# Kernel optimization log

Hardware: AMD Instinct MI355X
Metric: run time of the kernel (lower is better)

## Reference

```python
import jax, jax.numpy as jnp
import numpy as np

HIDDEN = 1024
HEADS = 16
HEAD_DIM = HIDDEN // HEADS
GAMMA = 0.5
B, S = 2, 2048


def setup_inputs() -> dict:
    key = jax.random.key(0)
    ks = jax.random.split(key, 9)
    sc = 1.0 / np.sqrt(HIDDEN)
    x = jax.random.normal(ks[0], (B, S, HIDDEN), dtype=jnp.float32)
    attn_mask = jnp.zeros((S, S), dtype=bool)  # True = masked; all-False here
    Wq = jax.random.normal(ks[1], (HIDDEN, HIDDEN), dtype=jnp.float32) * sc
    bq = jnp.zeros((HIDDEN,), dtype=jnp.float32)
    Wk = jax.random.normal(ks[2], (HIDDEN, HIDDEN), dtype=jnp.float32) * sc
    bk = jnp.zeros((HIDDEN,), dtype=jnp.float32)
    Wv = jax.random.normal(ks[3], (HIDDEN, HIDDEN), dtype=jnp.float32) * sc
    bv = jnp.zeros((HIDDEN,), dtype=jnp.float32)
    Wo = jax.random.normal(ks[4], (HIDDEN, HIDDEN), dtype=jnp.float32) * sc
    bo = jnp.zeros((HIDDEN,), dtype=jnp.float32)
    return {"x": x, "attn_mask": attn_mask, "Wq": Wq, "bq": bq,
            "Wk": Wk, "bk": bk, "Wv": Wv, "bv": bv, "Wo": Wo, "bo": bo}


def reference(x, attn_mask, Wq, bq, Wk, bk, Wv, bv, Wo, bo):
    Bn, Sn, _ = x.shape
    # projections (torch Linear: x @ W.T + b), reshape to [B, H, S, Dh]
    def proj(W, b):
        y = x @ W.T + b
        return y.reshape(Bn, Sn, HEADS, HEAD_DIM).transpose(0, 2, 1, 3)
    q, k, v = proj(Wq, bq), proj(Wk, bk), proj(Wv, bv)
    scores = jnp.einsum('bhqd,bhkd->bhqk', q, k) / np.sqrt(HEAD_DIM)
    # diversity bias: cosine similarity of raw x (F.normalize eps=1e-12)
    normed = x / jnp.maximum(jnp.linalg.norm(x, axis=-1, keepdims=True), 1e-12)
    sim = jnp.einsum('bqd,bkd->bqk', normed, normed)
    scores = scores - GAMMA * sim[:, None, :, :]
    scores = jnp.where(attn_mask[None, None, :, :], -jnp.inf, scores)
    probs = jax.nn.softmax(scores, axis=-1)
    ctx = jnp.einsum('bhqk,bhkd->bhqd', probs, v)
    ctx = ctx.transpose(0, 2, 1, 3).reshape(Bn, Sn, HIDDEN)
    return ctx @ Wo.T + bo
```

## Files before the change

kernel.cpp:

```cpp
#include <hip/hip_runtime.h>

#define HID 1024
#define SEQ 2048
#define NB 2
#define NH 16
#define HD 64

#define C1 0.1803368801111204f
#define C2 0.7213475204444817f

typedef __attribute__((ext_vector_type(8))) short bf16x8;
typedef __attribute__((ext_vector_type(8))) unsigned short u16x8;
typedef __attribute__((ext_vector_type(4))) float f32x4;

__device__ __forceinline__ unsigned short f2bf(float f) {
  unsigned u = __builtin_bit_cast(unsigned, f);
  u += 0x7fffu + ((u >> 16) & 1u);
  return (unsigned short)(u >> 16);
}
__device__ __forceinline__ float bf2f(unsigned short u) {
  return __builtin_bit_cast(float, ((unsigned)u) << 16);
}

#define GLOAD16(gsrc, ldst)                                                     \
  __builtin_amdgcn_global_load_lds(                                             \
      (const __attribute__((address_space(1))) void*)(gsrc),                    \
      (__attribute__((address_space(3))) void*)(ldst), 16, 0, 0)

__global__ __launch_bounds__(256) void convert_w_kernel(
    const float* __restrict__ Wq, const float* __restrict__ Wk,
    const float* __restrict__ Wv, const float* __restrict__ Wo,
    unsigned short* __restrict__ Wb) {
  int i = blockIdx.x * 256 + threadIdx.x;
  const int per = (HID * HID) / 8;
  int m = i / per;
  const float* sp = (m == 0) ? Wq : (m == 1) ? Wk : (m == 2) ? Wv : Wo;
  int j = (i - m * per) * 8;
  const float4* p = reinterpret_cast<const float4*>(sp + j);
  float4 a = p[0], b = p[1];
  u16x8 o;
  o[0] = f2bf(a.x); o[1] = f2bf(a.y); o[2] = f2bf(a.z); o[3] = f2bf(a.w);
  o[4] = f2bf(b.x); o[5] = f2bf(b.y); o[6] = f2bf(b.z); o[7] = f2bf(b.w);
  *reinterpret_cast<u16x8*>(Wb + (size_t)i * 8) = o;
}

__global__ __launch_bounds__(256) void rownorm_kernel(
    const float* __restrict__ x, unsigned short* __restrict__ xb,
    unsigned short* __restrict__ nxb) {
  int row = blockIdx.x, tid = threadIdx.x;
  const float4 v = reinterpret_cast<const float4*>(x + (size_t)row * HID)[tid];
  float ss = v.x * v.x + v.y * v.y + v.z * v.z + v.w * v.w;
#pragma unroll
  for (int off = 32; off; off >>= 1) ss += __shfl_xor(ss, off, 64);
  __shared__ float wsum[4];
  if ((tid & 63) == 0) wsum[tid >> 6] = ss;
  __syncthreads();
  float tot = wsum[0] + wsum[1] + wsum[2] + wsum[3];
  float inv = 1.0f / fmaxf(sqrtf(tot), 1e-12f);
  ushort4 a, b;
  a.x = f2bf(v.x); a.y = f2bf(v.y); a.z = f2bf(v.z); a.w = f2bf(v.w);
  b.x = f2bf(v.x * inv); b.y = f2bf(v.y * inv);
  b.z = f2bf(v.z * inv); b.w = f2bf(v.w * inv);
  reinterpret_cast<ushort4*>(xb  + (size_t)row * HID)[tid] = a;
  reinterpret_cast<ushort4*>(nxb + (size_t)row * HID)[tid] = b;
}

template <int MODE>
__global__ __launch_bounds__(256) void gemm_nt(
    const unsigned short* __restrict__ A, long strideA,
    const unsigned short* __restrict__ B, long strideB,
    void* __restrict__ Cv, long strideC, int ldc,
    int M, int N, int K,
    const float* __restrict__ b0, const float* __restrict__ b1,
    const float* __restrict__ b2, const unsigned char* __restrict__ mask) {
  __shared__ __align__(16) unsigned short As[128 * 32];
  __shared__ __align__(16) unsigned short Bs[128 * 32];
  int tid = threadIdx.x, lane = tid & 63, wid = tid >> 6;
  int g = lane >> 4, lr = lane & 15;
  int wr = wid >> 1, wc = wid & 1;
  int m0 = blockIdx.y * 128, n0 = blockIdx.x * 128;
  const unsigned short* Ab = A + (size_t)blockIdx.z * strideA
      + (size_t)(m0 + wid * 32 + (lane >> 2)) * K + (lane & 3) * 8;
  const unsigned short* Bb = B + (size_t)blockIdx.z * strideB
      + (size_t)(n0 + wid * 32 + (lane >> 2)) * K + (lane & 3) * 8;
  unsigned short* la = As + wid * 1024;
  unsigned short* lb = Bs + wid * 1024;
  f32x4 acc[4][4] = {};
  for (int k0 = 0; k0 < K; k0 += 32) {
    GLOAD16(Ab + k0, la);
    GLOAD16(Ab + 16 * K + k0, la + 512);
    GLOAD16(Bb + k0, lb);
    GLOAD16(Bb + 16 * K + k0, lb + 512);
    __syncthreads();
    bf16x8 af[4], bfr[4];
#pragma unroll
    for (int i = 0; i < 4; i++) {
      af[i]  = *reinterpret_cast<const bf16x8*>(&As[(wr * 64 + i * 16 + lr) * 32 + g * 8]);
      bfr[i] = *reinterpret_cast<const bf16x8*>(&Bs[(wc * 64 + i * 16 + lr) * 32 + g * 8]);
    }
#pragma unroll
    for (int i = 0; i < 4; i++)
#pragma unroll
      for (int j = 0; j < 4; j++)
        acc[i][j] = __builtin_amdgcn_mfma_f32_16x16x32_bf16(af[i], bfr[j], acc[i][j], 0, 0, 0);
    __syncthreads();
  }
#pragma unroll
  for (int i = 0; i < 4; i++)
#pragma unroll
    for (int j = 0; j < 4; j++) {
      int col = n0 + wc * 64 + j * 16 + lr;
#pragma unroll
      for (int r = 0; r < 4; r++) {
        int row = m0 + wr * 64 + i * 16 + 4 * g + r;
        float v = acc[i][j][r];
        if (MODE == 0) {
          const float* bp = (col < 1024) ? b0 : (col < 2048 ? b1 : b2);
          v += bp[col & 1023];
          ((unsigned short*)Cv)[(size_t)blockIdx.z * strideC + (size_t)row * ldc + col] = f2bf(v);
        } else if (MODE == 1) {
          float t = -C2 * v + (mask[(size_t)row * N + col] ? -1e30f : 0.0f);
          ((unsigned short*)Cv)[(size_t)blockIdx.z * strideC + (size_t)row * ldc + col] = f2bf(t);
        } else {
          v += b0[col];
          ((float*)Cv)[(size_t)blockIdx.z * strideC + (size_t)row * ldc + col] = v;
        }
      }
    }
}

__global__ __launch_bounds__(256, 4) void flash_kernel(
    const unsigned short* __restrict__ QKV,
    const unsigned short* __restrict__ D2,
    unsigned short* __restrict__ ctxb) {
  int h = blockIdx.x, qt = blockIdx.y, b = blockIdx.z;
  int tid = threadIdx.x, wid = tid >> 6, lane = tid & 63;
  int g = lane >> 4, lr = lane & 15;
  __shared__ __align__(16) unsigned short Ks[2][64 * 64];
  __shared__ __align__(16) unsigned short Vt[2][64 * 64];
  const size_t ld = 3 * HID;
  const size_t bS = (size_t)b * SEQ;
  const int qbase = qt * 64 + wid * 16;

  const unsigned short* qp = QKV + (bS + qbase + lr) * ld + h * HD + g * 8;
  bf16x8 qf0 = *reinterpret_cast<const bf16x8*>(qp);
  bf16x8 qf1 = *reinterpret_cast<const bf16x8*>(qp + 32);

  const int p0 = wid * 16 + (lane >> 3);
  const int key0 = ((p0 >> 5) & 1) * 32 + (((p0 >> 2) & 3) << 3)
                 + ((p0 >> 4) & 1) * 4 + (p0 & 3);
  const unsigned short* gK0 = QKV + (bS + key0) * ld + HID + h * HD
                              + (((lane & 7) ^ (lane >> 3)) << 3);
  const unsigned short* gK1 = gK0 + 16 * ld;

  const int vr0 = tid >> 3, ch = tid & 7;
  const unsigned short* gV0 = QKV + (bS + vr0) * ld + 2 * HID + h * HD + (ch << 3);
  const unsigned short* gV1 = gV0 + 32 * ld;
  const int kr3 = vr0 & 7;
  const int kb0v = vr0 >> 3, kb1v = kb0v + 4;
  const int vtbase = ch * 512 + kr3;
  const int pre0 = (kb0v ^ ch) & 7, pre1 = (kb1v ^ ch) & 7;

  const unsigned short* bD = D2 + (size_t)b * SEQ * SEQ
                             + (size_t)(qbase + lr) * SEQ + 8 * g;

  GLOAD16(gK0, &Ks[0][wid * 1024]);
  GLOAD16(gK1, &Ks[0][wid * 1024 + 512]);
  {
    u16x8 v0 = *reinterpret_cast<const u16x8*>(gV0);
    u16x8 v1 = *reinterpret_cast<const u16x8*>(gV1);
#pragma unroll
    for (int i = 0; i < 8; i++) {
      Vt[0][vtbase + i * 64 + ((pre0 ^ i) << 3)] = v0[i];
      Vt[0][vtbase + i * 64 + ((pre1 ^ i) << 3)] = v1[i];
    }
  }
  ushort4 bvc[4];
  bvc[0] = *reinterpret_cast<const ushort4*>(bD + 0);
  bvc[1] = *reinterpret_cast<const ushort4*>(bD + 4);
  bvc[2] = *reinterpret_cast<const ushort4*>(bD + 32);
  bvc[3] = *reinterpret_cast<const ushort4*>(bD + 36);
  __syncthreads();

  f32x4 acc[4] = {};
  f32x4 rsacc = {};
  const int kb0 = lr * 64 + ((g ^ (lr & 7)) << 3);
  bf16x8 ones;
#pragma unroll
  for (int i = 0; i < 8; i++) ones[i] = 0x3F80;

  for (int kt = 0; kt < 32; ++kt) {
    const int cb = kt & 1;
    const unsigned short* ks = &Ks[cb][0];
    const unsigned short* vt = &Vt[cb][0];
    u16x8 vv0 = {}, vv1 = {};
    ushort4 bvn[4];
    if (kt < 31) {
      GLOAD16(gK0 + (size_t)(kt + 1) * 64 * ld, &Ks[cb ^ 1][wid * 1024]);
      GLOAD16(gK1 + (size_t)(kt + 1) * 64 * ld, &Ks[cb ^ 1][wid * 1024 + 512]);
      vv0 = *reinterpret_cast<const u16x8*>(gV0 + (size_t)(kt + 1) * 64 * ld);
      vv1 = *reinterpret_cast<const u16x8*>(gV1 + (size_t)(kt + 1) * 64 * ld);
      const unsigned short* bn = bD + (kt + 1) * 64;
      bvn[0] = *reinterpret_cast<const ushort4*>(bn + 0);
      bvn[1] = *reinterpret_cast<const ushort4*>(bn + 4);
      bvn[2] = *reinterpret_cast<const ushort4*>(bn + 32);
      bvn[3] = *reinterpret_cast<const ushort4*>(bn + 36);
    }

    f32x4 s[4];
    __builtin_amdgcn_s_setprio(1);
#pragma unroll
    for (int kc = 0; kc < 4; kc++) {
      bf16x8 kf0 = *reinterpret_cast<const bf16x8*>(ks + kc * 1024 + kb0);
      bf16x8 kf1 = *reinterpret_cast<const bf16x8*>(ks + kc * 1024 + (kb0 ^ 32));
      f32x4 z = {};
      z = __builtin_amdgcn_mfma_f32_16x16x32_bf16(kf0, qf0, z, 0, 0, 0);
      s[kc] = __builtin_amdgcn_mfma_f32_16x16x32_bf16(kf1, qf1, z, 0, 0, 0);
    }
    __builtin_amdgcn_s_setprio(0);

    bf16x8 pa[2];
#pragma unroll
    for (int c2 = 0; c2 < 2; c2++) {
      float p0f = exp2f(fmaf(s[2 * c2][0], C1, bf2f(bvc[2 * c2].x)));
      float p1f = exp2f(fmaf(s[2 * c2][1], C1, bf2f(bvc[2 * c2].y)));
      float p2f = exp2f(fmaf(s[2 * c2][2], C1, bf2f(bvc[2 * c2].z)));
      float p3f = exp2f(fmaf(s[2 * c2][3], C1, bf2f(bvc[2 * c2].w)));
      float p4f = exp2f(fmaf(s[2 * c2 + 1][0], C1, bf2f(bvc[2 * c2 + 1].x)));
      float p5f = exp2f(fmaf(s[2 * c2 + 1][1], C1, bf2f(bvc[2 * c2 + 1].y)));
      float p6f = exp2f(fmaf(s[2 * c2 + 1][2], C1, bf2f(bvc[2 * c2 + 1].z)));
      float p7f = exp2f(fmaf(s[2 * c2 + 1][3], C1, bf2f(bvc[2 * c2 + 1].w)));
      uint4 W;
      W.x = __builtin_amdgcn_perm(__builtin_bit_cast(unsigned, p1f),
                                  __builtin_bit_cast(unsigned, p0f), 0x07060302u);
      W.y = __builtin_amdgcn_perm(__builtin_bit_cast(unsigned, p3f),
                                  __builtin_bit_cast(unsigned, p2f), 0x07060302u);
      W.z = __builtin_amdgcn_perm(__builtin_bit_cast(unsigned, p5f),
                                  __builtin_bit_cast(unsigned, p4f), 0x07060302u);
      W.w = __builtin_amdgcn_perm(__builtin_bit_cast(unsigned, p7f),
                                  __builtin_bit_cast(unsigned, p6f), 0x07060302u);
      pa[c2] = __builtin_bit_cast(bf16x8, W);
    }

    __builtin_amdgcn_s_setprio(1);
#pragma unroll
    for (int c2 = 0; c2 < 2; c2++) {
      rsacc = __builtin_amdgcn_mfma_f32_16x16x32_bf16(pa[c2], ones, rsacc, 0, 0, 0);
#pragma unroll
      for (int df = 0; df < 4; df++) {
        int blk = ((4 * c2 + g) ^ (lr & 7) ^ ((df * 2 + (lr >> 3)) & 7)) & 7;
        bf16x8 vf = *reinterpret_cast<const bf16x8*>(vt + (df * 16 + lr) * 64 + (blk << 3));
        acc[df] = __builtin_amdgcn_mfma_f32_16x16x32_bf16(pa[c2], vf, acc[df], 0, 0, 0);
      }
    }
    __builtin_amdgcn_s_setprio(0);

    if (kt < 31) {
#pragma unroll
      for (int i = 0; i < 8; i++) {
        Vt[cb ^ 1][vtbase + i * 64 + ((pre0 ^ i) << 3)] = vv0[i];
        Vt[cb ^ 1][vtbase + i * 64 + ((pre1 ^ i) << 3)] = vv1[i];
      }
      bvc[0] = bvn[0]; bvc[1] = bvn[1]; bvc[2] = bvn[2]; bvc[3] = bvn[3];
    }
    __syncthreads();
  }
  float l0 = 1.0f / rsacc[0], l1 = 1.0f / rsacc[1];
  float l2 = 1.0f / rsacc[2], l3 = 1.0f / rsacc[3];
  unsigned short* op = ctxb + (bS + qbase + 4 * g) * HID + h * HD + lr;
#pragma unroll
  for (int df = 0; df < 4; df++) {
    op[0 * HID + df * 16] = f2bf(acc[df][0] * l0);
    op[1 * HID + df * 16] = f2bf(acc[df][1] * l1);
    op[2 * HID + df * 16] = f2bf(acc[df][2] * l2);
    op[3 * HID + df * 16] = f2bf(acc[df][3] * l3);
  }
}

extern "C" void kernel_launch(void* const* d_in, const int* in_sizes, int n_in,
                              void* d_out, int out_size, void* d_ws, size_t ws_size,
                              hipStream_t stream) {
  const float* x = (const float*)d_in[0];
  const unsigned char* mask = (const unsigned char*)d_in[1];
  const float* Wq = (const float*)d_in[2];
  const float* bq = (const float*)d_in[3];
  const float* Wk = (const float*)d_in[4];
  const float* bk = (const float*)d_in[5];
  const float* Wv = (const float*)d_in[6];
  const float* bv = (const float*)d_in[7];
  const float* Wo = (const float*)d_in[8];
  const float* bo = (const float*)d_in[9];
  float* out = (float*)d_out;

  char* ws = (char*)d_ws;
  const size_t MiB = 1024 * 1024;
  unsigned short* xb  = (unsigned short*)(ws + 0 * MiB);
  unsigned short* nxb = (unsigned short*)(ws + 8 * MiB);
  unsigned short* Wb  = (unsigned short*)(ws + 16 * MiB);
  unsigned short* QKV = (unsigned short*)(ws + 24 * MiB);
  unsigned short* D2  = (unsigned short*)(ws + 48 * MiB);
  unsigned short* ctx = (unsigned short*)(ws + 64 * MiB);

  convert_w_kernel<<<2048, 256, 0, stream>>>(Wq, Wk, Wv, Wo, Wb);
  rownorm_kernel<<<NB * SEQ, 256, 0, stream>>>(x, xb, nxb);
  gemm_nt<0><<<dim3(24, 32, 1), 256, 0, stream>>>(
      xb, 0, Wb, 0, QKV, 0, 3 * HID, NB * SEQ, 3 * HID, HID, bq, bk, bv, nullptr);
  gemm_nt<1><<<dim3(16, 16, 2), 256, 0, stream>>>(
      nxb, (long)SEQ * HID, nxb, (long)SEQ * HID, D2, (long)SEQ * SEQ, SEQ,
      SEQ, SEQ, HID, nullptr, nullptr, nullptr, mask);
  flash_kernel<<<dim3(NH, SEQ / 64, NB), 256, 0, stream>>>(QKV, D2, ctx);
  gemm_nt<2><<<dim3(8, 32, 1), 256, 0, stream>>>(
      ctx, 0, Wb + (size_t)3 * HID * HID, 0, out, 0, HID, NB * SEQ, HID, HID,
      bo, nullptr, nullptr, nullptr);
}
```

Measured before the change: 194.5 us.

## Produce V pre-transposed via separate GEMM and load it asynchronously in flash

The fused QKV projection is split into a QK GEMM and a separate GEMM mode that computes V transposed (Wv·xᵀ with row bias) into a [HID, B*S] layout. The flash kernel then fills its V tile with the same direct global-to-LDS async loads used for K, instead of register loads followed by scalar scattered LDS transposition writes. This removes per-element LDS stores and register pressure in the inner loop. In exchange it adds an extra kernel launch and a transposed-output GEMM with strided 2-byte stores.

```diff
diff --git a/kernel.cpp b/kernel.cpp
--- a/kernel.cpp
+++ b/kernel.cpp
@@ -115,22 +115,26 @@
         int row = m0 + wr * 64 + i * 16 + 4 * g + r;
         float v = acc[i][j][r];
         if (MODE == 0) {
-          const float* bp = (col < 1024) ? b0 : (col < 2048 ? b1 : b2);
+          const float* bp = (col < 1024) ? b0 : b1;
           v += bp[col & 1023];
           ((unsigned short*)Cv)[(size_t)blockIdx.z * strideC + (size_t)row * ldc + col] = f2bf(v);
         } else if (MODE == 1) {
           float t = -C2 * v + (mask[(size_t)row * N + col] ? -1e30f : 0.0f);
           ((unsigned short*)Cv)[(size_t)blockIdx.z * strideC + (size_t)row * ldc + col] = f2bf(t);
-        } else {
+        } else if (MODE == 2) {
           v += b0[col];
           ((float*)Cv)[(size_t)blockIdx.z * strideC + (size_t)row * ldc + col] = v;
+        } else {
+          v += b0[row];
+          ((unsigned short*)Cv)[(size_t)blockIdx.z * strideC + (size_t)row * ldc + col] = f2bf(v);
         }
       }
     }
 }
 
 __global__ __launch_bounds__(256, 4) void flash_kernel(
-    const unsigned short* __restrict__ QKV,
+    const unsigned short* __restrict__ QK,
+    const unsigned short* __restrict__ VT,
     const unsigned short* __restrict__ D2,
     unsigned short* __restrict__ ctxb) {
   int h = blockIdx.x, qt = blockIdx.y, b = blockIdx.z;
@@ -138,43 +142,32 @@
   int g = lane >> 4, lr = lane & 15;
   __shared__ __align__(16) unsigned short Ks[2][64 * 64];
   __shared__ __align__(16) unsigned short Vt[2][64 * 64];
-  const size_t ld = 3 * HID;
+  const size_t ld = 2 * HID;
   const size_t bS = (size_t)b * SEQ;
   const int qbase = qt * 64 + wid * 16;
 
-  const unsigned short* qp = QKV + (bS + qbase + lr) * ld + h * HD + g * 8;
+  const unsigned short* qp = QK + (bS + qbase + lr) * ld + h * HD + g * 8;
   bf16x8 qf0 = *reinterpret_cast<const bf16x8*>(qp);
   bf16x8 qf1 = *reinterpret_cast<const bf16x8*>(qp + 32);
 
   const int p0 = wid * 16 + (lane >> 3);
   const int key0 = ((p0 >> 5) & 1) * 32 + (((p0 >> 2) & 3) << 3)
                  + ((p0 >> 4) & 1) * 4 + (p0 & 3);
-  const unsigned short* gK0 = QKV + (bS + key0) * ld + HID + h * HD
+  const unsigned short* gK0 = QK + (bS + key0) * ld + HID + h * HD
                               + (((lane & 7) ^ (lane >> 3)) << 3);
   const unsigned short* gK1 = gK0 + 16 * ld;
 
-  const int vr0 = tid >> 3, ch = tid & 7;
-  const unsigned short* gV0 = QKV + (bS + vr0) * ld + 2 * HID + h * HD + (ch << 3);
-  const unsigned short* gV1 = gV0 + 32 * ld;
-  const int kr3 = vr0 & 7;
-  const int kb0v = vr0 >> 3, kb1v = kb0v + 4;
-  const int vtbase = ch * 512 + kr3;
-  const int pre0 = (kb0v ^ ch) & 7, pre1 = (kb1v ^ ch) & 7;
+  const unsigned short* gV0 = VT + (size_t)(h * HD + wid * 16 + (lane >> 3)) * (2 * SEQ)
+                              + bS + (((lane & 7) ^ (lane >> 3)) << 3);
+  const unsigned short* gV1 = gV0 + (size_t)8 * (2 * SEQ);
 
   const unsigned short* bD = D2 + (size_t)b * SEQ * SEQ
                              + (size_t)(qbase + lr) * SEQ + 8 * g;
 
   GLOAD16(gK0, &Ks[0][wid * 1024]);
   GLOAD16(gK1, &Ks[0][wid * 1024 + 512]);
-  {
-    u16x8 v0 = *reinterpret_cast<const u16x8*>(gV0);
-    u16x8 v1 = *reinterpret_cast<const u16x8*>(gV1);
-#pragma unroll
-    for (int i = 0; i < 8; i++) {
-      Vt[0][vtbase + i * 64 + ((pre0 ^ i) << 3)] = v0[i];
-      Vt[0][vtbase + i * 64 + ((pre1 ^ i) << 3)] = v1[i];
-    }
-  }
+  GLOAD16(gV0, &Vt[0][wid * 1024]);
+  GLOAD16(gV1, &Vt[0][wid * 1024 + 512]);
   ushort4 bvc[4];
   bvc[0] = *reinterpret_cast<const ushort4*>(bD + 0);
   bvc[1] = *reinterpret_cast<const ushort4*>(bD + 4);
@@ -193,13 +186,12 @@
     const int cb = kt & 1;
     const unsigned short* ks = &Ks[cb][0];
     const unsigned short* vt = &Vt[cb][0];
-    u16x8 vv0 = {}, vv1 = {};
     ushort4 bvn[4];
     if (kt < 31) {
       GLOAD16(gK0 + (size_t)(kt + 1) * 64 * ld, &Ks[cb ^ 1][wid * 1024]);
       GLOAD16(gK1 + (size_t)(kt + 1) * 64 * ld, &Ks[cb ^ 1][wid * 1024 + 512]);
-      vv0 = *reinterpret_cast<const u16x8*>(gV0 + (size_t)(kt + 1) * 64 * ld);
-      vv1 = *reinterpret_cast<const u16x8*>(gV1 + (size_t)(kt + 1) * 64 * ld);
+      GLOAD16(gV0 + (kt + 1) * 64, &Vt[cb ^ 1][wid * 1024]);
+      GLOAD16(gV1 + (kt + 1) * 64, &Vt[cb ^ 1][wid * 1024 + 512]);
       const unsigned short* bn = bD + (kt + 1) * 64;
       bvn[0] = *reinterpret_cast<const ushort4*>(bn + 0);
       bvn[1] = *reinterpret_cast<const ushort4*>(bn + 4);
@@ -248,19 +240,14 @@
       rsacc = __builtin_amdgcn_mfma_f32_16x16x32_bf16(pa[c2], ones, rsacc, 0, 0, 0);
 #pragma unroll
       for (int df = 0; df < 4; df++) {
-        int blk = ((4 * c2 + g) ^ (lr & 7) ^ ((df * 2 + (lr >> 3)) & 7)) & 7;
-        bf16x8 vf = *reinterpret_cast<const bf16x8*>(vt + (df * 16 + lr) * 64 + (blk << 3));
+        bf16x8 vf = *reinterpret_cast<const bf16x8*>(
+            vt + (df * 16 + lr) * 64 + (((4 * c2 + g) ^ (lr & 7)) << 3));
         acc[df] = __builtin_amdgcn_mfma_f32_16x16x32_bf16(pa[c2], vf, acc[df], 0, 0, 0);
       }
     }
     __builtin_amdgcn_s_setprio(0);
 
     if (kt < 31) {
-#pragma unroll
-      for (int i = 0; i < 8; i++) {
-        Vt[cb ^ 1][vtbase + i * 64 + ((pre0 ^ i) << 3)] = vv0[i];
-        Vt[cb ^ 1][vtbase + i * 64 + ((pre1 ^ i) << 3)] = vv1[i];
-      }
       bvc[0] = bvn[0]; bvc[1] = bvn[1]; bvc[2] = bvn[2]; bvc[3] = bvn[3];
     }
     __syncthreads();
@@ -297,18 +284,22 @@
   unsigned short* xb  = (unsigned short*)(ws + 0 * MiB);
   unsigned short* nxb = (unsigned short*)(ws + 8 * MiB);
   unsigned short* Wb  = (unsigned short*)(ws + 16 * MiB);
-  unsigned short* QKV = (unsigned short*)(ws + 24 * MiB);
+  unsigned short* QK  = (unsigned short*)(ws + 24 * MiB);
+  unsigned short* VT  = (unsigned short*)(ws + 40 * MiB);
   unsigned short* D2  = (unsigned short*)(ws + 48 * MiB);
   unsigned short* ctx = (unsigned short*)(ws + 64 * MiB);
 
   convert_w_kernel<<<2048, 256, 0, stream>>>(Wq, Wk, Wv, Wo, Wb);
   rownorm_kernel<<<NB * SEQ, 256, 0, stream>>>(x, xb, nxb);
-  gemm_nt<0><<<dim3(24, 32, 1), 256, 0, stream>>>(
-      xb, 0, Wb, 0, QKV, 0, 3 * HID, NB * SEQ, 3 * HID, HID, bq, bk, bv, nullptr);
+  gemm_nt<0><<<dim3(16, 32, 1), 256, 0, stream>>>(
+      xb, 0, Wb, 0, QK, 0, 2 * HID, NB * SEQ, 2 * HID, HID, bq, bk, nullptr, nullptr);
+  gemm_nt<3><<<dim3(32, 8, 1), 256, 0, stream>>>(
+      Wb + (size_t)2 * HID * HID, 0, xb, 0, VT, 0, 2 * SEQ, HID, NB * SEQ, HID,
+      bv, nullptr, nullptr, nullptr);
   gemm_nt<1><<<dim3(16, 16, 2), 256, 0, stream>>>(
       nxb, (long)SEQ * HID, nxb, (long)SEQ * HID, D2, (long)SEQ * SEQ, SEQ,
       SEQ, SEQ, HID, nullptr, nullptr, nullptr, mask);
-  flash_kernel<<<dim3(NH, SEQ / 64, NB), 256, 0, stream>>>(QKV, D2, ctx);
+  flash_kernel<<<dim3(NH, SEQ / 64, NB), 256, 0, stream>>>(QK, VT, D2, ctx);
   gemm_nt<2><<<dim3(8, 32, 1), 256, 0, stream>>>(
       ctx, 0, Wb + (size_t)3 * HID * HID, 0, out, 0, HID, NB * SEQ, HID, HID,
       bo, nullptr, nullptr, nullptr);
```

New measurement: 204.2 us. 1.05x slower.
